# Optimization experiments

Hardware: AMD Instinct MI355X
Metric: run time of the kernel (lower is better)

The kernel has to match this reference:

```python
import jax, jax.numpy as jnp
import numpy as np

GRIDS = ((16, 16, 16), (32, 16, 8), (8, 32, 16))  # prod == 4096 == N_p for each scale
PAIRS = ((0, 1), (0, 2), (1, 2))
KVOL = 27.0  # 3x3x3 kernel, count_include_pad=True -> always divide by 27


def _avg_pool3(x):
    # x: [B, C, d, h, w]; avg_pool3d kernel 3, stride 1, pad 1 (shape preserving)
    s = jax.lax.reduce_window(
        x, 0.0, jax.lax.add,
        window_dimensions=(1, 1, 3, 3, 3),
        window_strides=(1, 1, 1, 1, 1),
        padding=((0, 0), (0, 0), (1, 1), (1, 1), (1, 1)))
    return s / KVOL


def _window(feat, grid):
    # feat: [B, N, D] -> raw reshape into [B, D, d, h, w] (layout-mixing, faithful to torch .reshape)
    B, N, D = feat.shape
    x = feat.reshape(B, -1, *grid)
    p = _avg_pool3(x)
    return p.reshape(B, p.shape[1], -1).transpose(0, 2, 1)  # [B, N, D]


def setup_inputs() -> dict:
    key = jax.random.key(0)
    ks = jax.random.split(key, 8)
    B, N, D = 8, 4096, 512
    e0 = jax.random.normal(ks[0], (B, N, D), jnp.float32)
    e1 = jax.random.normal(ks[1], (B, N, D), jnp.float32)
    e2 = jax.random.normal(ks[2], (B, N, D), jnp.float32)
    W1 = jax.random.normal(ks[3], (3, 2 * D, D), jnp.float32) * 0.02
    b1 = jnp.zeros((3, D), jnp.float32)
    W2 = jax.random.normal(ks[4], (3, D, 1), jnp.float32) * 0.02
    b2 = jnp.zeros((3, 1), jnp.float32)
    gamma = jnp.ones((D,), jnp.float32)
    beta = jnp.zeros((D,), jnp.float32)
    Wf = jax.random.normal(ks[5], (D, D), jnp.float32) * 0.02
    bf = jnp.zeros((D,), jnp.float32)
    return dict(e0=e0, e1=e1, e2=e2, W1=W1, b1=b1, W2=W2, b2=b2,
                gamma=gamma, beta=beta, Wf=Wf, bf=bf)


def reference(e0, e1, e2, W1, b1, W2, b2, gamma, beta, Wf, bf):
    embeds = (e0, e1, e2)
    windows = [_window(embeds[s], GRIDS[s]) for s in range(3)]  # each [B, N, D]
    matched = []
    for k, (i, j) in enumerate(PAIRS):
        def mlp(c):
            h = jax.nn.relu(jnp.einsum('bne,ed->bnd', c, W1[k]) + b1[k])
            return jnp.einsum('bnd,do->bno', h, W2[k]) + b2[k]  # [B, N, 1]
        cij = jnp.concatenate([windows[i], windows[j]], axis=-1)  # [B, N, 2D]
        cji = jnp.concatenate([windows[j], windows[i]], axis=-1)
        aij = jax.nn.softmax(mlp(cij), axis=1)
        aji = jax.nn.softmax(mlp(cji), axis=1)
        matched.append(jnp.sum(aij * embeds[j], axis=1, keepdims=True))  # [B, 1, D]
        matched.append(jnp.sum(aji * embeds[i], axis=1, keepdims=True))
    fused = jnp.concatenate(list(embeds) + matched, axis=1).mean(axis=1)  # [B, D]
    mu = fused.mean(axis=-1, keepdims=True)
    var = fused.var(axis=-1, keepdims=True)
    ln = (fused - mu) / jnp.sqrt(var + 1e-5) * gamma + beta
    return ln @ Wf + bf  # [B, D]
```

## Files before the change

### kernel.cpp

```cpp
#include <hip/hip_runtime.h>
#include <hip/hip_bf16.h>

typedef unsigned short u16;
typedef __bf16 bf16x8 __attribute__((ext_vector_type(8)));
typedef float f32x4 __attribute__((ext_vector_type(4)));


static __device__ __forceinline__ u16 f2bf(float f) {
  unsigned u = __builtin_bit_cast(unsigned, f);
  unsigned r = (u + 0x7FFFu + ((u >> 16) & 1u)) >> 16;
  return (u16)r;
}

__global__ __launch_bounds__(512) void k_poolpack(const float* __restrict__ e0,
                                                  const float* __restrict__ e1,
                                                  const float* __restrict__ e2,
                                                  u16* __restrict__ packA,
                                                  int b0, int nb) {
  __shared__ __align__(16) float v[4096];
  __shared__ __align__(16) float t1[4096];
  __shared__ __align__(16) u16 outp[16384];
  int bx = blockIdx.x;
  int cg4 = bx & 127;
  int q = bx >> 7;
  int scale = q / nb;
  int lb = q - scale * nb;
  int b = b0 + lb;
  const float* eptr = scale == 0 ? e0 : (scale == 1 ? e1 : e2);
  const int LW = (scale == 0) ? 4 : (scale == 1 ? 3 : 4);
  const int LHW = (scale == 0) ? 8 : (scale == 1 ? 7 : 9);
  const int w = 1 << LW, hw = 1 << LHW;
  const int h = hw >> LW;
  const int dep = 4096 >> LHW;
  int t = threadIdx.x;
  int c0 = cg4 * 4;
  for (int ci = 0; ci < 4; ++ci) {
    const float* src = eptr + (size_t)b * 2097152 + (size_t)(c0 + ci) * 4096;
    ((float4*)v)[t] = ((const float4*)src)[t];
    ((float4*)v)[t + 512] = ((const float4*)src)[t + 512];
    __syncthreads();
    for (int j = 0; j < 8; ++j) {
      int s = t + j * 512;
      int x = s & (w - 1);
      float sum = v[s];
      if (x > 0) sum += v[s - 1];
      if (x < w - 1) sum += v[s + 1];
      t1[s] = sum;
    }
    __syncthreads();
    for (int j = 0; j < 8; ++j) {
      int s = t + j * 512;
      int y = (s >> LW) & (h - 1);
      float sum = t1[s];
      if (y > 0) sum += t1[s - w];
      if (y < h - 1) sum += t1[s + w];
      v[s] = sum;
    }
    __syncthreads();
    for (int j = 0; j < 8; ++j) {
      int s = t + j * 512;
      int z = s >> LHW;
      float sum = v[s];
      if (z > 0) sum += v[s - hw];
      if (z < dep - 1) sum += v[s + hw];
      outp[s * 4 + ci] = f2bf(sum * (1.0f / 27.0f));
    }
    __syncthreads();
  }
  int cb = c0 >> 5;
  int hi = (c0 >> 3) & 3;
  int eh = (c0 >> 2) & 1;
  size_t blk = (size_t)(lb * 3 + scale) * 2097152;
  for (int k2 = 0; k2 < 8; ++k2) {
    int s = t + k2 * 512;
    int2 val = *(const int2*)&outp[s * 4];
    size_t dst = blk + ((size_t)(s >> 4) * 16 + cb) * 512 +
                 (size_t)(hi * 16 + (s & 15)) * 8 + eh * 4;
    *(int2*)(packA + dst) = val;
  }
}

__global__ __launch_bounds__(64) void k_packW(const float* __restrict__ W1,
                                              u16* __restrict__ W1p) {
  int u = blockIdx.x;
  int kb = u & 31;
  int nb_ = (u >> 5) & 31;
  int kp = u >> 10;
  int l = threadIdx.x;
  int m = l & 15, hi = l >> 4;
  u16 tmp[8];
  for (int e = 0; e < 8; ++e) {
    int kg = kb * 32 + hi * 8 + e;
    tmp[e] = f2bf(W1[((size_t)kp * 1024 + kg) * 512 + nb_ * 16 + m]);
  }
  *(int4*)(W1p + ((size_t)u * 64 + l) * 8) = *(int4*)tmp;
}

__global__ __launch_bounds__(512) void k_gemm(const u16* __restrict__ packA,
                                              const u16* __restrict__ W1p,
                                              const float* __restrict__ b1,
                                              const float* __restrict__ W2,
                                              float* __restrict__ logits,
                                              int b0, int nb) {
  __shared__ __align__(16) u16 abuf[2][16384];
  __shared__ float red[512];
  int per = gridDim.x >> 3;
  int logical = (blockIdx.x & 7) * per + (blockIdx.x >> 3);
  int dir = logical % 6;
  int group = logical / 6;
  int mt = group & 63;
  int lb = group >> 6;
  int b = b0 + lb;
  int kp = dir >> 1, sw = dir & 1;
  const int PI[3] = {0, 0, 1}, PJ[3] = {1, 2, 2};
  int pi = PI[kp], pj = PJ[kp];
  int first = sw ? pj : pi;
  int second = sw ? pi : pj;
  int t = threadIdx.x;
  int w = t >> 6;
  int l = t & 63;
  const u16* Abase1 = packA + (size_t)(lb * 3 + first) * 2097152 + (size_t)mt * 32768;
  const u16* Abase2 = packA + (size_t)(lb * 3 + second) * 2097152 + (size_t)mt * 32768;
  const u16* Bp = W1p + ((size_t)kp * 32 + w * 4) * 32 * 512 + (size_t)l * 8;

  f32x4 acc[4][4];
  for (int a = 0; a < 4; ++a)
    for (int n = 0; n < 4; ++n) acc[a][n] = (f32x4){0.f, 0.f, 0.f, 0.f};

#define STAGE(BUFI, CHUNK)                                                        \
  do {                                                                            \
    const u16* P_ = ((CHUNK) < 2) ? Abase1 : Abase2;                              \
    const int cc0_ = ((CHUNK) & 1) * 8;                                           \
    for (int qi = 0; qi < 4; ++qi) {                                              \
      int q_ = w * 4 + qi;                                                        \
      const u16* g_ = P_ + (size_t)(q_ >> 3) * 8192 +                             \
                      (size_t)(cc0_ + (q_ & 7)) * 512 + (size_t)l * 8;            \
      u16* lp_ = &abuf[BUFI][q_ * 512];                                           \
      __builtin_amdgcn_global_load_lds(                                           \
          (const __attribute__((address_space(1))) void*)g_,                      \
          (__attribute__((address_space(3))) void*)lp_, 16, 0, 0);                \
    }                                                                             \
  } while (0)

#define COMPUTE(BUFI, CHUNK)                                                      \
  do {                                                                            \
    _Pragma("unroll")                                                             \
    for (int kk = 0; kk < 8; ++kk) {                                              \
      int ks_ = (CHUNK) * 8 + kk;                                                 \
      bf16x8 af[4], bfr[4];                                                       \
      for (int mi = 0; mi < 4; ++mi)                                              \
        af[mi] = *(const bf16x8*)&abuf[BUFI][(mi * 8 + kk) * 512 + l * 8];        \
      for (int ni = 0; ni < 4; ++ni)                                              \
        bfr[ni] = *(const bf16x8*)(Bp + (size_t)(ni * 32 + ks_) * 512);           \
      for (int mi = 0; mi < 4; ++mi)                                              \
        for (int ni = 0; ni < 4; ++ni)                                            \
          acc[mi][ni] = __builtin_amdgcn_mfma_f32_16x16x32_bf16(                  \
              af[mi], bfr[ni], acc[mi][ni], 0, 0, 0);                             \
    }                                                                             \
  } while (0)

  STAGE(0, 0);
  STAGE(1, 1);
  asm volatile("s_waitcnt vmcnt(4)" ::: "memory");
  __builtin_amdgcn_sched_barrier(0);
  __builtin_amdgcn_s_barrier();
  COMPUTE(0, 0);
  __builtin_amdgcn_s_barrier();
  STAGE(0, 2);
  asm volatile("s_waitcnt vmcnt(4)" ::: "memory");
  __builtin_amdgcn_sched_barrier(0);
  __builtin_amdgcn_s_barrier();
  COMPUTE(1, 1);
  __builtin_amdgcn_s_barrier();
  STAGE(1, 3);
  asm volatile("s_waitcnt vmcnt(4)" ::: "memory");
  __builtin_amdgcn_sched_barrier(0);
  __builtin_amdgcn_s_barrier();
  COMPUTE(0, 2);
  __builtin_amdgcn_s_barrier();
  asm volatile("s_waitcnt vmcnt(0)" ::: "memory");
  __builtin_amdgcn_sched_barrier(0);
  __builtin_amdgcn_s_barrier();
  COMPUTE(1, 3);
#undef STAGE
#undef COMPUTE

  int m = l & 15, hi = l >> 4;
  float w2v[4], b1v[4];
  for (int ni = 0; ni < 4; ++ni) {
    int n = w * 64 + ni * 16 + m;
    w2v[ni] = W2[kp * 512 + n];
    b1v[ni] = b1[kp * 512 + n];
  }
  float rs[4][4];
  for (int mi = 0; mi < 4; ++mi)
    for (int r = 0; r < 4; ++r) {
      float s = 0.f;
      for (int ni = 0; ni < 4; ++ni) {
        float h = acc[mi][ni][r] + b1v[ni];
        s += fmaxf(h, 0.f) * w2v[ni];
      }
      float vv = s;
      vv += __shfl_xor(vv, 1);
      vv += __shfl_xor(vv, 2);
      vv += __shfl_xor(vv, 4);
      vv += __shfl_xor(vv, 8);
      rs[mi][r] = vv;
    }
  if (m == 0) {
    for (int mi = 0; mi < 4; ++mi)
      for (int r = 0; r < 4; ++r)
        red[w * 64 + mi * 16 + hi * 4 + r] = rs[mi][r];
  }
  __syncthreads();
  if (t < 64) {
    float s = 0.f;
    for (int ww = 0; ww < 8; ++ww) s += red[ww * 64 + t];
    logits[((size_t)dir * 8 + b) * 4096 + mt * 64 + t] = s;
  }
}

__global__ __launch_bounds__(256) void k_softmax(float* __restrict__ logits) {
  __shared__ __align__(16) float buf[4096];
  __shared__ float wred[4];
  int row = blockIdx.x;
  float* p = logits + (size_t)row * 4096;
  int t = threadIdx.x;
  float lmax = -1e30f;
  for (int j = 0; j < 4; ++j) {
    float4 v = ((const float4*)p)[t + j * 256];
    v.x = fmaxf(fminf(v.x, 1e4f), -1e4f);
    v.y = fmaxf(fminf(v.y, 1e4f), -1e4f);
    v.z = fmaxf(fminf(v.z, 1e4f), -1e4f);
    v.w = fmaxf(fminf(v.w, 1e4f), -1e4f);
    ((float4*)buf)[t + j * 256] = v;
    lmax = fmaxf(lmax, fmaxf(fmaxf(v.x, v.y), fmaxf(v.z, v.w)));
  }
  for (int off = 1; off < 64; off <<= 1) lmax = fmaxf(lmax, __shfl_xor(lmax, off));
  if ((t & 63) == 0) wred[t >> 6] = lmax;
  __syncthreads();
  float gmax = fmaxf(fmaxf(wred[0], wred[1]), fmaxf(wred[2], wred[3]));
  __syncthreads();
  float lsum = 0.f;
  for (int j = 0; j < 16; ++j) {
    int s = t + j * 256;
    float ex = expf(buf[s] - gmax);
    buf[s] = ex;
    lsum += ex;
  }
  for (int off = 1; off < 64; off <<= 1) lsum += __shfl_xor(lsum, off);
  if ((t & 63) == 0) wred[t >> 6] = lsum;
  __syncthreads();
  float inv = 1.f / (wred[0] + wred[1] + wred[2] + wred[3]);
  for (int j = 0; j < 4; ++j) {
    int i4 = t + j * 256;
    float4 v = ((const float4*)buf)[i4];
    v.x *= inv; v.y *= inv; v.z *= inv; v.w *= inv;
    ((float4*)p)[i4] = v;
  }
}

__global__ void k_zero(float* __restrict__ p, int n) {
  int i = blockIdx.x * 256 + threadIdx.x;
  if (i < n) p[i] = 0.f;
}

__global__ __launch_bounds__(256) void k_matched(const float* __restrict__ e0,
                                                 const float* __restrict__ e1,
                                                 const float* __restrict__ e2,
                                                 const float* __restrict__ wts,
                                                 float* __restrict__ fused) {
  __shared__ float lw[384];
  int bx = blockIdx.x;
  int nc = bx & 63;
  int b = bx >> 6;
  int n0 = nc * 64;
  int t = threadIdx.x;
  for (int idx = t; idx < 384; idx += 256) {
    int dir = idx >> 6, nn = idx & 63;
    lw[idx] = wts[((size_t)dir * 8 + b) * 4096 + n0 + nn];
  }
  __syncthreads();
  size_t base = (size_t)b * 2097152 + (size_t)n0 * 512;
  const float2* p0 = (const float2*)(e0 + base) + t;
  const float2* p1 = (const float2*)(e1 + base) + t;
  const float2* p2 = (const float2*)(e2 + base) + t;
  float2 tot = {0.f, 0.f};
  float2 m0 = {0, 0}, m1 = {0, 0}, m2 = {0, 0}, m3 = {0, 0}, m4 = {0, 0}, m5 = {0, 0};
  for (int nn = 0; nn < 64; ++nn) {
    float2 v0 = p0[nn * 256];
    float2 v1 = p1[nn * 256];
    float2 v2 = p2[nn * 256];
    tot.x += v0.x + v1.x + v2.x;
    tot.y += v0.y + v1.y + v2.y;
    float w0 = lw[0 * 64 + nn], w1 = lw[1 * 64 + nn], w2 = lw[2 * 64 + nn];
    float w3 = lw[3 * 64 + nn], w4 = lw[4 * 64 + nn], w5 = lw[5 * 64 + nn];
    m0.x += w0 * v1.x; m0.y += w0 * v1.y;
    m1.x += w1 * v0.x; m1.y += w1 * v0.y;
    m2.x += w2 * v2.x; m2.y += w2 * v2.y;
    m3.x += w3 * v0.x; m3.y += w3 * v0.y;
    m4.x += w4 * v2.x; m4.y += w4 * v2.y;
    m5.x += w5 * v1.x; m5.y += w5 * v1.y;
  }
  float rx = tot.x + m0.x + m1.x + m2.x + m3.x + m4.x + m5.x;
  float ry = tot.y + m0.y + m1.y + m2.y + m3.y + m4.y + m5.y;
  atomicAdd(&fused[b * 512 + 2 * t], rx);
  atomicAdd(&fused[b * 512 + 2 * t + 1], ry);
}

__global__ __launch_bounds__(512) void k_final(const float* __restrict__ fused,
                                               const float* __restrict__ gamma,
                                               const float* __restrict__ beta,
                                               const float* __restrict__ Wf,
                                               const float* __restrict__ bfv,
                                               float* __restrict__ out) {
  __shared__ float lnv[512];
  __shared__ float sred[16];
  __shared__ float pred[4][128];
  int bx = blockIdx.x;
  int db = bx & 3, b = bx >> 2;
  int t = threadIdx.x;
  float f = fused[b * 512 + t] * (1.0f / 12294.0f);
  float s1 = f, s2 = f * f;
  for (int off = 1; off < 64; off <<= 1) {
    s1 += __shfl_xor(s1, off);
    s2 += __shfl_xor(s2, off);
  }
  if ((t & 63) == 0) {
    sred[(t >> 6) * 2] = s1;
    sred[(t >> 6) * 2 + 1] = s2;
  }
  __syncthreads();
  float S1 = 0.f, S2 = 0.f;
  for (int ww = 0; ww < 8; ++ww) {
    S1 += sred[ww * 2];
    S2 += sred[ww * 2 + 1];
  }
  float mu = S1 * (1.0f / 512.0f);
  float var = S2 * (1.0f / 512.0f) - mu * mu;
  float rstd = rsqrtf(var + 1e-5f);
  lnv[t] = (f - mu) * rstd * gamma[t] + beta[t];
  __syncthreads();
  int dt = t & 127, eq = t >> 7;
  int d = db * 128 + dt;
  float acc = 0.f;
  for (int e = eq * 128; e < eq * 128 + 128; ++e)
    acc += lnv[e] * Wf[(size_t)e * 512 + d];
  pred[eq][dt] = acc;
  __syncthreads();
  if (t < 128) {
    float r = pred[0][t] + pred[1][t] + pred[2][t] + pred[3][t] + bfv[db * 128 + t];
    out[b * 512 + db * 128 + t] = r;
  }
}

extern "C" void kernel_launch(void* const* d_in, const int* in_sizes, int n_in,
                              void* d_out, int out_size, void* d_ws, size_t ws_size,
                              hipStream_t stream) {
  const float* e0 = (const float*)d_in[0];
  const float* e1 = (const float*)d_in[1];
  const float* e2 = (const float*)d_in[2];
  const float* W1 = (const float*)d_in[3];
  const float* b1 = (const float*)d_in[4];
  const float* W2 = (const float*)d_in[5];
  const float* gamma = (const float*)d_in[7];
  const float* beta = (const float*)d_in[8];
  const float* Wf = (const float*)d_in[9];
  const float* bf = (const float*)d_in[10];

  char* ws = (char*)d_ws;
  float* fused = (float*)ws;
  float* logits = (float*)(ws + 16384);
  u16* W1p = (u16*)(ws + 802816);
  u16* packA = (u16*)(ws + 3948544);
  int nbat = 8;
  while (nbat > 1 && 3948544 + (size_t)nbat * 12582912 > ws_size) nbat >>= 1;

  hipLaunchKernelGGL(k_zero, dim3(16), dim3(256), 0, stream, fused, 4096);
  hipLaunchKernelGGL(k_packW, dim3(3072), dim3(64), 0, stream, W1, W1p);
  for (int b0 = 0; b0 < 8; b0 += nbat) {
    hipLaunchKernelGGL(k_poolpack, dim3(3 * nbat * 128), dim3(512), 0, stream,
                       e0, e1, e2, packA, b0, nbat);
    hipLaunchKernelGGL(k_gemm, dim3(6 * nbat * 64), dim3(512), 0, stream,
                       packA, W1p, b1, W2, logits, b0, nbat);
  }
  hipLaunchKernelGGL(k_softmax, dim3(48), dim3(256), 0, stream, logits);
  hipLaunchKernelGGL(k_matched, dim3(512), dim3(256), 0, stream, e0, e1, e2, logits, fused);
  hipLaunchKernelGGL(k_final, dim3(32), dim3(512), 0, stream, fused, gamma, beta, Wf, bf,
                     (float*)d_out);
}
```

Measured before the change: 563.5 us.

## Retile logits GEMM into 128x128 tiles with LDS-staged weights and atomic reduction

The GEMM kernel moves from 64-row tiles covering all 512 output columns, with weights read straight from global memory, to 128x128 output tiles using 256-thread blocks. The K dimension is walked over 32 double-buffered stages, and both A and W1 tiles are staged into LDS through global_load_lds. Because each block now produces only a partial sum over a quarter of the N columns, per-row logits are accumulated with atomicAdd, and the zero kernel is widened to clear the logits buffer as well. The aim is better operand reuse and occupancy (launch bounds 256,3). The cost is atomic traffic, float summation order that depends on execution order, and 4x more A reads across the N tiles.

```diff
diff --git a/kernel.cpp b/kernel.cpp
--- a/kernel.cpp
+++ b/kernel.cpp
@@ -96,20 +96,22 @@
   *(int4*)(W1p + ((size_t)u * 64 + l) * 8) = *(int4*)tmp;
 }
 
-__global__ __launch_bounds__(512) void k_gemm(const u16* __restrict__ packA,
-                                              const u16* __restrict__ W1p,
-                                              const float* __restrict__ b1,
-                                              const float* __restrict__ W2,
-                                              float* __restrict__ logits,
-                                              int b0, int nb) {
-  __shared__ __align__(16) u16 abuf[2][16384];
-  __shared__ float red[512];
+__global__ __launch_bounds__(256, 3) void k_gemm(const u16* __restrict__ packA,
+                                                 const u16* __restrict__ W1p,
+                                                 const float* __restrict__ b1,
+                                                 const float* __restrict__ W2,
+                                                 float* __restrict__ logits,
+                                                 int b0, int nb) {
+  __shared__ __align__(16) u16 abuf[2][4096];
+  __shared__ __align__(16) u16 bbuf[2][4096];
+  __shared__ float red[2][128];
   int per = gridDim.x >> 3;
   int logical = (blockIdx.x & 7) * per + (blockIdx.x >> 3);
-  int dir = logical % 6;
-  int group = logical / 6;
-  int mt = group & 63;
-  int lb = group >> 6;
+  int nt = logical & 3;
+  int mt = (logical >> 2) & 31;
+  int rest = logical >> 7;
+  int lb = rest % nb;
+  int dir = rest / nb;
   int b = b0 + lb;
   int kp = dir >> 1, sw = dir & 1;
   const int PI[3] = {0, 0, 1}, PJ[3] = {1, 2, 2};
@@ -119,80 +121,78 @@
   int t = threadIdx.x;
   int w = t >> 6;
   int l = t & 63;
-  const u16* Abase1 = packA + (size_t)(lb * 3 + first) * 2097152 + (size_t)mt * 32768;
-  const u16* Abase2 = packA + (size_t)(lb * 3 + second) * 2097152 + (size_t)mt * 32768;
-  const u16* Bp = W1p + ((size_t)kp * 32 + w * 4) * 32 * 512 + (size_t)l * 8;
+  int wr = w & 1, wc = w >> 1;
+  const u16* Abase1 = packA + (size_t)(lb * 3 + first) * 2097152;
+  const u16* Abase2 = packA + (size_t)(lb * 3 + second) * 2097152;
 
   f32x4 acc[4][4];
   for (int a = 0; a < 4; ++a)
     for (int n = 0; n < 4; ++n) acc[a][n] = (f32x4){0.f, 0.f, 0.f, 0.f};
 
-#define STAGE(BUFI, CHUNK)                                                        \
+#define STAGE(BUFI, T)                                                            \
   do {                                                                            \
-    const u16* P_ = ((CHUNK) < 2) ? Abase1 : Abase2;                              \
-    const int cc0_ = ((CHUNK) & 1) * 8;                                           \
-    for (int qi = 0; qi < 4; ++qi) {                                              \
-      int q_ = w * 4 + qi;                                                        \
-      const u16* g_ = P_ + (size_t)(q_ >> 3) * 8192 +                             \
-                      (size_t)(cc0_ + (q_ & 7)) * 512 + (size_t)l * 8;            \
-      u16* lp_ = &abuf[BUFI][q_ * 512];                                           \
+    const u16* P_ = ((T) < 16) ? Abase1 : Abase2;                                 \
+    int cb_ = (T) & 15;                                                           \
+    for (int r_ = 0; r_ < 2; ++r_) {                                              \
+      int u_ = r_ * 4 + w;                                                        \
+      const u16* g_ = P_ + ((size_t)((mt * 8 + u_) * 16 + cb_)) * 512 +           \
+                      (size_t)l * 8;                                              \
       __builtin_amdgcn_global_load_lds(                                           \
           (const __attribute__((address_space(1))) void*)g_,                      \
-          (__attribute__((address_space(3))) void*)lp_, 16, 0, 0);                \
+          (__attribute__((address_space(3))) void*)&abuf[BUFI][u_ * 512],         \
+          16, 0, 0);                                                              \
+    }                                                                             \
+    for (int r_ = 0; r_ < 2; ++r_) {                                              \
+      int u_ = r_ * 4 + w;                                                        \
+      const u16* g_ = W1p + ((size_t)((kp * 32 + nt * 8 + u_) * 32 + (T))) * 512 +\
+                      (size_t)l * 8;                                              \
+      __builtin_amdgcn_global_load_lds(                                           \
+          (const __attribute__((address_space(1))) void*)g_,                      \
+          (__attribute__((address_space(3))) void*)&bbuf[BUFI][u_ * 512],         \
+          16, 0, 0);                                                              \
     }                                                                             \
   } while (0)
 
-#define COMPUTE(BUFI, CHUNK)                                                      \
+#define COMPUTE(BUFI)                                                             \
   do {                                                                            \
+    bf16x8 af[4], bfr[4];                                                         \
     _Pragma("unroll")                                                             \
-    for (int kk = 0; kk < 8; ++kk) {                                              \
-      int ks_ = (CHUNK) * 8 + kk;                                                 \
-      bf16x8 af[4], bfr[4];                                                       \
-      for (int mi = 0; mi < 4; ++mi)                                              \
-        af[mi] = *(const bf16x8*)&abuf[BUFI][(mi * 8 + kk) * 512 + l * 8];        \
+    for (int mi = 0; mi < 4; ++mi)                                                \
+      af[mi] = *(const bf16x8*)&abuf[BUFI][(wr * 4 + mi) * 512 + l * 8];          \
+    _Pragma("unroll")                                                             \
+    for (int ni = 0; ni < 4; ++ni)                                                \
+      bfr[ni] = *(const bf16x8*)&bbuf[BUFI][(wc * 4 + ni) * 512 + l * 8];         \
+    _Pragma("unroll")                                                             \
+    for (int mi = 0; mi < 4; ++mi)                                                \
+      _Pragma("unroll")                                                           \
       for (int ni = 0; ni < 4; ++ni)                                              \
-        bfr[ni] = *(const bf16x8*)(Bp + (size_t)(ni * 32 + ks_) * 512);           \
-      for (int mi = 0; mi < 4; ++mi)                                              \
-        for (int ni = 0; ni < 4; ++ni)                                            \
-          acc[mi][ni] = __builtin_amdgcn_mfma_f32_16x16x32_bf16(                  \
-              af[mi], bfr[ni], acc[mi][ni], 0, 0, 0);                             \
-    }                                                                             \
+        acc[mi][ni] = __builtin_amdgcn_mfma_f32_16x16x32_bf16(                    \
+            af[mi], bfr[ni], acc[mi][ni], 0, 0, 0);                               \
   } while (0)
 
   STAGE(0, 0);
-  STAGE(1, 1);
-  asm volatile("s_waitcnt vmcnt(4)" ::: "memory");
-  __builtin_amdgcn_sched_barrier(0);
-  __builtin_amdgcn_s_barrier();
-  COMPUTE(0, 0);
-  __builtin_amdgcn_s_barrier();
-  STAGE(0, 2);
-  asm volatile("s_waitcnt vmcnt(4)" ::: "memory");
-  __builtin_amdgcn_sched_barrier(0);
-  __builtin_amdgcn_s_barrier();
-  COMPUTE(1, 1);
-  __builtin_amdgcn_s_barrier();
-  STAGE(1, 3);
-  asm volatile("s_waitcnt vmcnt(4)" ::: "memory");
-  __builtin_amdgcn_sched_barrier(0);
-  __builtin_amdgcn_s_barrier();
-  COMPUTE(0, 2);
-  __builtin_amdgcn_s_barrier();
+  for (int tt = 0; tt < 31; ++tt) {
+    STAGE((tt + 1) & 1, tt + 1);
+    asm volatile("s_waitcnt vmcnt(4)" ::: "memory");
+    __builtin_amdgcn_sched_barrier(0);
+    __builtin_amdgcn_s_barrier();
+    COMPUTE(tt & 1);
+    __builtin_amdgcn_s_barrier();
+  }
   asm volatile("s_waitcnt vmcnt(0)" ::: "memory");
   __builtin_amdgcn_sched_barrier(0);
   __builtin_amdgcn_s_barrier();
-  COMPUTE(1, 3);
+  COMPUTE(1);
 #undef STAGE
 #undef COMPUTE
 
   int m = l & 15, hi = l >> 4;
   float w2v[4], b1v[4];
   for (int ni = 0; ni < 4; ++ni) {
-    int n = w * 64 + ni * 16 + m;
+    int n = nt * 128 + wc * 64 + ni * 16 + m;
     w2v[ni] = W2[kp * 512 + n];
     b1v[ni] = b1[kp * 512 + n];
   }
-  float rs[4][4];
   for (int mi = 0; mi < 4; ++mi)
     for (int r = 0; r < 4; ++r) {
       float s = 0.f;
@@ -205,18 +205,12 @@
       vv += __shfl_xor(vv, 2);
       vv += __shfl_xor(vv, 4);
       vv += __shfl_xor(vv, 8);
-      rs[mi][r] = vv;
+      if (m == 0) red[wc][wr * 64 + mi * 16 + hi * 4 + r] = vv;
     }
-  if (m == 0) {
-    for (int mi = 0; mi < 4; ++mi)
-      for (int r = 0; r < 4; ++r)
-        red[w * 64 + mi * 16 + hi * 4 + r] = rs[mi][r];
-  }
-  __syncthreads();
-  if (t < 64) {
-    float s = 0.f;
-    for (int ww = 0; ww < 8; ++ww) s += red[ww * 64 + t];
-    logits[((size_t)dir * 8 + b) * 4096 + mt * 64 + t] = s;
+  __syncthreads();
+  if (t < 128) {
+    float s = red[0][t] + red[1][t];
+    atomicAdd(&logits[((size_t)dir * 8 + b) * 4096 + mt * 128 + t], s);
   }
 }
 
@@ -376,12 +370,12 @@
   int nbat = 8;
   while (nbat > 1 && 3948544 + (size_t)nbat * 12582912 > ws_size) nbat >>= 1;
 
-  hipLaunchKernelGGL(k_zero, dim3(16), dim3(256), 0, stream, fused, 4096);
+  hipLaunchKernelGGL(k_zero, dim3(784), dim3(256), 0, stream, fused, 200704);
   hipLaunchKernelGGL(k_packW, dim3(3072), dim3(64), 0, stream, W1, W1p);
   for (int b0 = 0; b0 < 8; b0 += nbat) {
     hipLaunchKernelGGL(k_poolpack, dim3(3 * nbat * 128), dim3(512), 0, stream,
                        e0, e1, e2, packA, b0, nbat);
-    hipLaunchKernelGGL(k_gemm, dim3(6 * nbat * 64), dim3(512), 0, stream,
+    hipLaunchKernelGGL(k_gemm, dim3(768 * nbat), dim3(256), 0, stream,
                        packA, W1p, b1, W2, logits, b0, nbat);
   }
   hipLaunchKernelGGL(k_softmax, dim3(48), dim3(256), 0, stream, logits);
```

Result: faster. 537.9 us (-4.5%).
